# Kernel tuning notes

Measured on AMD Instinct MI355X. Metric: run time of the kernel, lower is better.

The kernel has to match this reference:

```python
import jax, jax.numpy as jnp
import numpy as np

POOL = (7, 7)


def crop_and_resize(fmap, boxes, box_idx, ph, pw):
    """tf.image.crop_and_resize (bilinear) for normalized boxes (y1,x1,y2,x2).
    fmap: [B,H,W,C], boxes: [N,4], box_idx: [N] int32 -> [N,ph,pw,C]."""
    H, W = fmap.shape[1], fmap.shape[2]
    dt = fmap.dtype
    y1, x1, y2, x2 = boxes[:, 0], boxes[:, 1], boxes[:, 2], boxes[:, 3]
    ty = jnp.arange(ph, dtype=dt) / (ph - 1)
    tx = jnp.arange(pw, dtype=dt) / (pw - 1)
    ys = (y1[:, None] + ty[None, :] * (y2 - y1)[:, None]) * (H - 1)  # [N,ph]
    xs = (x1[:, None] + tx[None, :] * (x2 - x1)[:, None]) * (W - 1)  # [N,pw]
    y0f = jnp.clip(jnp.floor(ys), 0.0, H - 1)
    x0f = jnp.clip(jnp.floor(xs), 0.0, W - 1)
    y0 = y0f.astype(jnp.int32)
    x0 = x0f.astype(jnp.int32)
    y1i = jnp.minimum(y0 + 1, H - 1)
    x1i = jnp.minimum(x0 + 1, W - 1)
    wy = (ys - y0f)[:, :, None, None]  # [N,ph,1,1]
    wx = (xs - x0f)[:, None, :, None]  # [N,1,pw,1]
    b = box_idx[:, None, None]
    v00 = fmap[b, y0[:, :, None], x0[:, None, :]]  # [N,ph,pw,C]
    v01 = fmap[b, y0[:, :, None], x1i[:, None, :]]
    v10 = fmap[b, y1i[:, :, None], x0[:, None, :]]
    v11 = fmap[b, y1i[:, :, None], x1i[:, None, :]]
    top = v00 + (v01 - v00) * wx
    bot = v10 + (v11 - v10) * wx
    return top + (bot - top) * wy


def setup_inputs() -> dict:
    key = jax.random.key(0)
    k1, k2, k3, k4, kp2, kp3, kp4, kp5 = jax.random.split(key, 8)
    B, N, C = 1, 1000, 256
    y1 = jax.random.uniform(k1, (B, N)) * 0.7
    x1 = jax.random.uniform(k2, (B, N)) * 0.7
    h = jax.random.uniform(k3, (B, N)) * 0.4 + 0.01
    w = jax.random.uniform(k4, (B, N)) * 0.4 + 0.01
    ROIboxes = jnp.stack([y1, x1, jnp.minimum(y1 + h, 1.0), jnp.minimum(x1 + w, 1.0)], axis=-1)
    meta = np.zeros((B, 93), np.float32)
    meta[:, 4:7] = [1024.0, 1024.0, 3.0]  # image_shape
    return {
        "ROIboxes": ROIboxes.astype(jnp.float32),
        "image_meta": jnp.asarray(meta),
        "P2": jax.random.normal(kp2, (B, 256, 256, C), jnp.float32),
        "P3": jax.random.normal(kp3, (B, 128, 128, C), jnp.float32),
        "P4": jax.random.normal(kp4, (B, 64, 64, C), jnp.float32),
        "P5": jax.random.normal(kp5, (B, 32, 32, C), jnp.float32),
    }


def reference(ROIboxes, image_meta, P2, P3, P4, P5):
    feature_maps = [P2, P3, P4, P5]
    B, N = ROIboxes.shape[0], ROIboxes.shape[1]
    boxes = jax.lax.stop_gradient(ROIboxes.reshape(-1, 4))  # [B*N,4]
    box_idx = jnp.repeat(jnp.arange(B, dtype=jnp.int32), N)
    image_shape = image_meta[0, 4:7]
    image_area = image_shape[0] * image_shape[1]
    h = boxes[:, 2] - boxes[:, 0]
    w = boxes[:, 3] - boxes[:, 1]
    roi_level = jnp.log2(jnp.sqrt(h * w) / (224.0 / jnp.sqrt(image_area)))
    roi_level = jnp.clip(4 + jnp.round(roi_level).astype(jnp.int32), 2, 5)  # [B*N]
    ph, pw = POOL
    C = P2.shape[-1]
    pooled = jnp.zeros((B * N, ph, pw, C), P2.dtype)
    for i, level in enumerate(range(2, 6)):
        p = crop_and_resize(feature_maps[i], boxes, box_idx, ph, pw)
        mask = (roi_level == level)[:, None, None, None]
        pooled = pooled + jnp.where(mask, p, 0.0)
    # Original gathers per-level then sorts back to original ROI order; the
    # masked-sum above produces the same per-ROI result in original order.
    return pooled[None]  # [1, B*N, ph, pw, C]
```

## Files before the change

### kernel.cpp

```cpp
#include <hip/hip_runtime.h>
#include <hip/hip_bf16.h>
#include <math.h>


#define CCH 256
#define PH 7
#define PW 7
#define NXCD 8

typedef float nat_float4 __attribute__((ext_vector_type(4)));

__global__ __launch_bounds__(256) void sort_boxes_kernel(
    const float* __restrict__ boxes, const float* __restrict__ meta,
    int* __restrict__ perm, int* __restrict__ keys, int total_boxes)
{
    __shared__ int hist[256];
    __shared__ int scan[256];
    int tid = threadIdx.x;
    hist[tid] = 0;
    __syncthreads();

    float area  = meta[4] * meta[5];
    float scale = 224.0f / sqrtf(area);

    for (int i = tid; i < total_boxes; i += 256) {
        float y1 = boxes[i * 4 + 0], x1 = boxes[i * 4 + 1];
        float y2 = boxes[i * 4 + 2], x2 = boxes[i * 4 + 3];
        int lvl = 4 + (int)rintf(log2f(sqrtf((y2 - y1) * (x2 - x1)) / scale));
        lvl = min(max(lvl, 2), 5);
        int yb = min(7, max(0, (int)((y1 + y2) * 4.0f)));
        int xb = min(7, max(0, (int)((x1 + x2) * 4.0f)));
        int key = ((lvl - 2) << 6) | (yb << 3) | xb;
        keys[i] = key;
        atomicAdd(&hist[key], 1);
    }
    __syncthreads();

    int v = hist[tid];
    scan[tid] = v;
    __syncthreads();
    #pragma unroll
    for (int d = 1; d < 256; d <<= 1) {
        int t = (tid >= d) ? scan[tid - d] : 0;
        __syncthreads();
        scan[tid] += t;
        __syncthreads();
    }
    hist[tid] = scan[tid] - v;
    __syncthreads();

    for (int i = tid; i < total_boxes; i += 256) {
        int key = keys[i];
        int pos = atomicAdd(&hist[key], 1);
        perm[pos] = i;
    }
}

__global__ __launch_bounds__(256, 4) void PyramidROIAlign_kernel(
    const float* __restrict__ boxes,
    const float* __restrict__ meta,
    const float* __restrict__ P2,
    const float* __restrict__ P3,
    const float* __restrict__ P4,
    const float* __restrict__ P5,
    const int*   __restrict__ perm,
    float* __restrict__ out,
    int total_boxes,
    int n_per_batch)
{
    int nwg = gridDim.x;
    int q = nwg / NXCD, r = nwg % NXCD;
    int xcd = blockIdx.x % NXCD;
    int off = blockIdx.x / NXCD;
    int bid = (xcd < r ? xcd * (q + 1) : r * (q + 1) + (xcd - r) * q) + off;

    int wid  = bid * 4 + (threadIdx.x >> 6);
    int lane = threadIdx.x & 63;
    if (wid >= total_boxes * PH) return;
    wid = __builtin_amdgcn_readfirstlane(wid);

    int spos = wid / PH;
    int py   = wid - spos * PH;
    int n    = perm[spos];
    n = __builtin_amdgcn_readfirstlane(n);

    float y1 = boxes[n * 4 + 0];
    float x1 = boxes[n * 4 + 1];
    float y2 = boxes[n * 4 + 2];
    float x2 = boxes[n * 4 + 3];

    float area  = meta[4] * meta[5];
    float scale = 224.0f / sqrtf(area);
    float lvlf  = log2f(sqrtf((y2 - y1) * (x2 - x1)) / scale);
    int level = 4 + (int)rintf(lvlf);
    level = min(max(level, 2), 5);

    const float* fmap;
    int H;
    switch (level) {
        case 2:  fmap = P2; H = 256; break;
        case 3:  fmap = P3; H = 128; break;
        case 4:  fmap = P4; H = 64;  break;
        default: fmap = P5; H = 32;  break;
    }
    int W = H;
    int b = n / n_per_batch;
    fmap += (size_t)b * H * W * CCH;

    float ty  = (float)py / (float)(PH - 1);
    float ys  = (y1 + ty * (y2 - y1)) * (float)(H - 1);
    float y0f = fminf(fmaxf(floorf(ys), 0.0f), (float)(H - 1));
    int   y0  = (int)y0f;
    int   y1r = min(y0 + 1, H - 1);
    float wy  = ys - y0f;

    int c = lane << 2;
    const float* row0 = fmap + (size_t)y0  * W * CCH + c;
    const float* row1 = fmap + (size_t)y1r * W * CCH + c;

    float* optr = out + ((size_t)n * (PH * PW) + py * PW) * CCH + c;

    #pragma unroll
    for (int px = 0; px < PW; ++px) {
        float tx  = (float)px / (float)(PW - 1);
        float xs  = (x1 + tx * (x2 - x1)) * (float)(W - 1);
        float x0f = fminf(fmaxf(floorf(xs), 0.0f), (float)(W - 1));
        int   x0  = (int)x0f;
        int   x1c = min(x0 + 1, W - 1);
        float wx  = xs - x0f;

        int o0 = x0  * CCH;
        int o1 = x1c * CCH;
        float4 v00 = *(const float4*)(row0 + o0);
        float4 v01 = *(const float4*)(row0 + o1);
        float4 v10 = *(const float4*)(row1 + o0);
        float4 v11 = *(const float4*)(row1 + o1);

        nat_float4 o;
        float top, bot;
        top = v00.x + (v01.x - v00.x) * wx;
        bot = v10.x + (v11.x - v10.x) * wx;
        o.x = top + (bot - top) * wy;
        top = v00.y + (v01.y - v00.y) * wx;
        bot = v10.y + (v11.y - v10.y) * wx;
        o.y = top + (bot - top) * wy;
        top = v00.z + (v01.z - v00.z) * wx;
        bot = v10.z + (v11.z - v10.z) * wx;
        o.z = top + (bot - top) * wy;
        top = v00.w + (v01.w - v00.w) * wx;
        bot = v10.w + (v11.w - v10.w) * wx;
        o.w = top + (bot - top) * wy;

        __builtin_nontemporal_store(o, (nat_float4*)(optr + px * CCH));
    }
}

extern "C" void kernel_launch(void* const* d_in, const int* in_sizes, int n_in,
                              void* d_out, int out_size, void* d_ws, size_t ws_size,
                              hipStream_t stream) {
    const float* boxes = (const float*)d_in[0];
    const float* meta  = (const float*)d_in[1];
    const float* P2    = (const float*)d_in[2];
    const float* P3    = (const float*)d_in[3];
    const float* P4    = (const float*)d_in[4];
    const float* P5    = (const float*)d_in[5];
    float* out = (float*)d_out;

    int total_boxes = in_sizes[0] / 4;
    int B = in_sizes[1] / 93;
    if (B < 1) B = 1;
    int n_per_batch = total_boxes / B;

    int* perm = (int*)d_ws;
    int* keys = perm + total_boxes;

    sort_boxes_kernel<<<1, 256, 0, stream>>>(boxes, meta, perm, keys, total_boxes);

    long total_waves = (long)total_boxes * PH;
    int blocks = (int)((total_waves + 3) / 4);

    PyramidROIAlign_kernel<<<blocks, 256, 0, stream>>>(
        boxes, meta, P2, P3, P4, P5, perm, out, total_boxes, n_per_batch);
}
```

Measured before the change: 29.05 us.

## Convert P3-P5 feature maps to bf16 before ROI bilinear sampling

Adds a per-call kernel that converts the P3, P4 and P5 feature maps to bf16 in workspace. The ROI-align kernel then gathers from those copies for levels 3-5 and keeps fp32 for P2. The intent is to halve gather bytes for the coarser levels. In exchange it pays for a full read and write pass over those maps every call, and it lowers input precision.

```diff
diff --git a/kernel.cpp b/kernel.cpp
--- a/kernel.cpp
+++ b/kernel.cpp
@@ -9,6 +9,35 @@
 #define NXCD 8
 
 typedef float nat_float4 __attribute__((ext_vector_type(4)));
+typedef unsigned short nat_ushort4 __attribute__((ext_vector_type(4)));
+
+__device__ __forceinline__ unsigned short f2bf(float f) {
+    unsigned u = __float_as_uint(f);
+    return (unsigned short)((u + 0x7fffu + ((u >> 16) & 1u)) >> 16);
+}
+__device__ __forceinline__ float bf_lo(unsigned x) { return __uint_as_float(x << 16); }
+__device__ __forceinline__ float bf_hi(unsigned x) { return __uint_as_float(x & 0xffff0000u); }
+
+__global__ __launch_bounds__(256) void convert_kernel(
+    const float* __restrict__ P3, const float* __restrict__ P4,
+    const float* __restrict__ P5,
+    unsigned short* __restrict__ B3, unsigned short* __restrict__ B4,
+    unsigned short* __restrict__ B5,
+    int n3_4, int n4_4, int n5_4)
+{
+    int total = n3_4 + n4_4 + n5_4;
+    int stride = gridDim.x * blockDim.x;
+    for (int i = blockIdx.x * blockDim.x + threadIdx.x; i < total; i += stride) {
+        const float* src; unsigned short* dst; int j = i;
+        if (j < n3_4) { src = P3; dst = B3; }
+        else if (j - n3_4 < n4_4) { j -= n3_4; src = P4; dst = B4; }
+        else { j -= n3_4 + n4_4; src = P5; dst = B5; }
+        float4 v = ((const float4*)src)[j];
+        nat_ushort4 o;
+        o.x = f2bf(v.x); o.y = f2bf(v.y); o.z = f2bf(v.z); o.w = f2bf(v.w);
+        ((nat_ushort4*)dst)[j] = o;
+    }
+}
 
 __global__ __launch_bounds__(256) void sort_boxes_kernel(
     const float* __restrict__ boxes, const float* __restrict__ meta,
@@ -50,50 +79,146 @@
     __syncthreads();
 
     for (int i = tid; i < total_boxes; i += 256) {
-        int key = keys[i];
-        int pos = atomicAdd(&hist[key], 1);
+        int pos = atomicAdd(&hist[keys[i]], 1);
         perm[pos] = i;
     }
 }
 
-__global__ __launch_bounds__(256, 4) void PyramidROIAlign_kernel(
-    const float* __restrict__ boxes,
-    const float* __restrict__ meta,
+#define BOX_PROLOGUE                                                          \
+    int nwg = gridDim.x;                                                      \
+    int q = nwg / NXCD, r = nwg % NXCD;                                       \
+    int xcd = blockIdx.x % NXCD;                                              \
+    int off = blockIdx.x / NXCD;                                              \
+    int bid = (xcd < r ? xcd * (q + 1) : r * (q + 1) + (xcd - r) * q) + off;  \
+    int wid  = bid * 4 + (threadIdx.x >> 6);                                  \
+    int lane = threadIdx.x & 63;                                              \
+    if (wid >= total_boxes * PH) return;                                      \
+    wid = __builtin_amdgcn_readfirstlane(wid);                                \
+    int spos = wid / PH;                                                      \
+    int py   = wid - spos * PH;                                               \
+    int n    = perm[spos];                                                    \
+    n = __builtin_amdgcn_readfirstlane(n);                                    \
+    float y1 = boxes[n * 4 + 0];                                              \
+    float x1 = boxes[n * 4 + 1];                                              \
+    float y2 = boxes[n * 4 + 2];                                              \
+    float x2 = boxes[n * 4 + 3];                                              \
+    float area  = meta[4] * meta[5];                                          \
+    float scale = 224.0f / sqrtf(area);                                       \
+    float lvlf  = log2f(sqrtf((y2 - y1) * (x2 - x1)) / scale);                \
+    int level = 4 + (int)rintf(lvlf);                                         \
+    level = min(max(level, 2), 5);
+
+#define INTERP_STORE(V00, V01, V10, V11)                                      \
+    {                                                                         \
+        nat_float4 o;                                                         \
+        float top, bot;                                                       \
+        top = V00.x + (V01.x - V00.x) * wx;                                   \
+        bot = V10.x + (V11.x - V10.x) * wx;                                   \
+        o.x = top + (bot - top) * wy;                                         \
+        top = V00.y + (V01.y - V00.y) * wx;                                   \
+        bot = V10.y + (V11.y - V10.y) * wx;                                   \
+        o.y = top + (bot - top) * wy;                                         \
+        top = V00.z + (V01.z - V00.z) * wx;                                   \
+        bot = V10.z + (V11.z - V10.z) * wx;                                   \
+        o.z = top + (bot - top) * wy;                                         \
+        top = V00.w + (V01.w - V00.w) * wx;                                   \
+        bot = V10.w + (V11.w - V10.w) * wx;                                   \
+        o.w = top + (bot - top) * wy;                                         \
+        __builtin_nontemporal_store(o, (nat_float4*)(optr + px * CCH));       \
+    }
+
+__global__ __launch_bounds__(256, 4) void PyramidROIAlign_bf16_kernel(
+    const float* __restrict__ boxes, const float* __restrict__ meta,
     const float* __restrict__ P2,
-    const float* __restrict__ P3,
-    const float* __restrict__ P4,
-    const float* __restrict__ P5,
-    const int*   __restrict__ perm,
-    float* __restrict__ out,
-    int total_boxes,
-    int n_per_batch)
+    const unsigned short* __restrict__ B3, const unsigned short* __restrict__ B4,
+    const unsigned short* __restrict__ B5,
+    const int* __restrict__ perm,
+    float* __restrict__ out, int total_boxes, int n_per_batch)
 {
-    int nwg = gridDim.x;
-    int q = nwg / NXCD, r = nwg % NXCD;
-    int xcd = blockIdx.x % NXCD;
-    int off = blockIdx.x / NXCD;
-    int bid = (xcd < r ? xcd * (q + 1) : r * (q + 1) + (xcd - r) * q) + off;
-
-    int wid  = bid * 4 + (threadIdx.x >> 6);
-    int lane = threadIdx.x & 63;
-    if (wid >= total_boxes * PH) return;
-    wid = __builtin_amdgcn_readfirstlane(wid);
-
-    int spos = wid / PH;
-    int py   = wid - spos * PH;
-    int n    = perm[spos];
-    n = __builtin_amdgcn_readfirstlane(n);
-
-    float y1 = boxes[n * 4 + 0];
-    float x1 = boxes[n * 4 + 1];
-    float y2 = boxes[n * 4 + 2];
-    float x2 = boxes[n * 4 + 3];
-
-    float area  = meta[4] * meta[5];
-    float scale = 224.0f / sqrtf(area);
-    float lvlf  = log2f(sqrtf((y2 - y1) * (x2 - x1)) / scale);
-    int level = 4 + (int)rintf(lvlf);
-    level = min(max(level, 2), 5);
+    BOX_PROLOGUE
+
+    int b = n / n_per_batch;
+    float* optr;
+    int c = lane << 2;
+
+    if (level == 2) {
+        const int H = 256, W = 256;
+        const float* fmap = P2 + (size_t)b * H * W * CCH;
+        float ty  = (float)py / (float)(PH - 1);
+        float ys  = (y1 + ty * (y2 - y1)) * (float)(H - 1);
+        float y0f = fminf(fmaxf(floorf(ys), 0.0f), (float)(H - 1));
+        int   y0  = (int)y0f;
+        int   y1r = min(y0 + 1, H - 1);
+        float wy  = ys - y0f;
+        const float* row0 = fmap + (size_t)y0  * W * CCH + c;
+        const float* row1 = fmap + (size_t)y1r * W * CCH + c;
+        optr = out + ((size_t)n * (PH * PW) + py * PW) * CCH + c;
+        #pragma unroll
+        for (int px = 0; px < PW; ++px) {
+            float tx  = (float)px / (float)(PW - 1);
+            float xs  = (x1 + tx * (x2 - x1)) * (float)(W - 1);
+            float x0f = fminf(fmaxf(floorf(xs), 0.0f), (float)(W - 1));
+            int   x0  = (int)x0f;
+            int   x1c = min(x0 + 1, W - 1);
+            float wx  = xs - x0f;
+            int o0 = x0  * CCH;
+            int o1 = x1c * CCH;
+            float4 v00 = *(const float4*)(row0 + o0);
+            float4 v01 = *(const float4*)(row0 + o1);
+            float4 v10 = *(const float4*)(row1 + o0);
+            float4 v11 = *(const float4*)(row1 + o1);
+            INTERP_STORE(v00, v01, v10, v11)
+        }
+    } else {
+        const unsigned short* bmap;
+        int H;
+        switch (level) {
+            case 3:  bmap = B3; H = 128; break;
+            case 4:  bmap = B4; H = 64;  break;
+            default: bmap = B5; H = 32;  break;
+        }
+        int W = H;
+        bmap += (size_t)b * H * W * CCH;
+        float ty  = (float)py / (float)(PH - 1);
+        float ys  = (y1 + ty * (y2 - y1)) * (float)(H - 1);
+        float y0f = fminf(fmaxf(floorf(ys), 0.0f), (float)(H - 1));
+        int   y0  = (int)y0f;
+        int   y1r = min(y0 + 1, H - 1);
+        float wy  = ys - y0f;
+        const unsigned short* br0 = bmap + (size_t)y0  * W * CCH + c;
+        const unsigned short* br1 = bmap + (size_t)y1r * W * CCH + c;
+        optr = out + ((size_t)n * (PH * PW) + py * PW) * CCH + c;
+        #pragma unroll
+        for (int px = 0; px < PW; ++px) {
+            float tx  = (float)px / (float)(PW - 1);
+            float xs  = (x1 + tx * (x2 - x1)) * (float)(W - 1);
+            float x0f = fminf(fmaxf(floorf(xs), 0.0f), (float)(W - 1));
+            int   x0  = (int)x0f;
+            int   x1c = min(x0 + 1, W - 1);
+            float wx  = xs - x0f;
+            int o0 = x0  * CCH;
+            int o1 = x1c * CCH;
+            uint2 u00 = *(const uint2*)(const void*)(br0 + o0);
+            uint2 u01 = *(const uint2*)(const void*)(br0 + o1);
+            uint2 u10 = *(const uint2*)(const void*)(br1 + o0);
+            uint2 u11 = *(const uint2*)(const void*)(br1 + o1);
+            nat_float4 v00 = { bf_lo(u00.x), bf_hi(u00.x), bf_lo(u00.y), bf_hi(u00.y) };
+            nat_float4 v01 = { bf_lo(u01.x), bf_hi(u01.x), bf_lo(u01.y), bf_hi(u01.y) };
+            nat_float4 v10 = { bf_lo(u10.x), bf_hi(u10.x), bf_lo(u10.y), bf_hi(u10.y) };
+            nat_float4 v11 = { bf_lo(u11.x), bf_hi(u11.x), bf_lo(u11.y), bf_hi(u11.y) };
+            INTERP_STORE(v00, v01, v10, v11)
+        }
+    }
+}
+
+__global__ __launch_bounds__(256, 4) void PyramidROIAlign_fp32_kernel(
+    const float* __restrict__ boxes, const float* __restrict__ meta,
+    const float* __restrict__ P2, const float* __restrict__ P3,
+    const float* __restrict__ P4, const float* __restrict__ P5,
+    const int* __restrict__ perm,
+    float* __restrict__ out, int total_boxes, int n_per_batch)
+{
+    BOX_PROLOGUE
 
     const float* fmap;
     int H;
@@ -117,7 +242,6 @@
     int c = lane << 2;
     const float* row0 = fmap + (size_t)y0  * W * CCH + c;
     const float* row1 = fmap + (size_t)y1r * W * CCH + c;
-
     float* optr = out + ((size_t)n * (PH * PW) + py * PW) * CCH + c;
 
     #pragma unroll
@@ -128,30 +252,13 @@
         int   x0  = (int)x0f;
         int   x1c = min(x0 + 1, W - 1);
         float wx  = xs - x0f;
-
         int o0 = x0  * CCH;
         int o1 = x1c * CCH;
         float4 v00 = *(const float4*)(row0 + o0);
         float4 v01 = *(const float4*)(row0 + o1);
         float4 v10 = *(const float4*)(row1 + o0);
         float4 v11 = *(const float4*)(row1 + o1);
-
-        nat_float4 o;
-        float top, bot;
-        top = v00.x + (v01.x - v00.x) * wx;
-        bot = v10.x + (v11.x - v10.x) * wx;
-        o.x = top + (bot - top) * wy;
-        top = v00.y + (v01.y - v00.y) * wx;
-        bot = v10.y + (v11.y - v10.y) * wx;
-        o.y = top + (bot - top) * wy;
-        top = v00.z + (v01.z - v00.z) * wx;
-        bot = v10.z + (v11.z - v10.z) * wx;
-        o.z = top + (bot - top) * wy;
-        top = v00.w + (v01.w - v00.w) * wx;
-        bot = v10.w + (v11.w - v10.w) * wx;
-        o.w = top + (bot - top) * wy;
-
-        __builtin_nontemporal_store(o, (nat_float4*)(optr + px * CCH));
+        INTERP_STORE(v00, v01, v10, v11)
     }
 }
 
@@ -171,14 +278,32 @@
     if (B < 1) B = 1;
     int n_per_batch = total_boxes / B;
 
+    int n3 = in_sizes[3], n4 = in_sizes[4], n5 = in_sizes[5];
+
     int* perm = (int*)d_ws;
     int* keys = perm + total_boxes;
+    size_t bfOff = (((size_t)2 * total_boxes * sizeof(int)) + 255) & ~(size_t)255;
+    size_t need = bfOff + (size_t)(n3 + n4 + n5) * sizeof(unsigned short);
+    bool use_bf16 = (ws_size >= need);
+
+    unsigned short* B3 = (unsigned short*)((char*)d_ws + bfOff);
+    unsigned short* B4 = B3 + n3;
+    unsigned short* B5 = B4 + n4;
 
     sort_boxes_kernel<<<1, 256, 0, stream>>>(boxes, meta, perm, keys, total_boxes);
 
     long total_waves = (long)total_boxes * PH;
     int blocks = (int)((total_waves + 3) / 4);
 
-    PyramidROIAlign_kernel<<<blocks, 256, 0, stream>>>(
-        boxes, meta, P2, P3, P4, P5, perm, out, total_boxes, n_per_batch);
-}
+    if (use_bf16) {
+        int tot4 = (n3 + n4 + n5) / 4;
+        int cblocks = min(2048, (tot4 + 255) / 256);
+        convert_kernel<<<cblocks, 256, 0, stream>>>(P3, P4, P5, B3, B4, B5,
+                                                    n3 / 4, n4 / 4, n5 / 4);
+        PyramidROIAlign_bf16_kernel<<<blocks, 256, 0, stream>>>(
+            boxes, meta, P2, B3, B4, B5, perm, out, total_boxes, n_per_batch);
+    } else {
+        PyramidROIAlign_fp32_kernel<<<blocks, 256, 0, stream>>>(
+            boxes, meta, P2, P3, P4, P5, perm, out, total_boxes, n_per_batch);
+    }
+}
```

After: 36.34 us. 25.1% more time.
